# Kernel optimization log

Hardware: AMD Instinct MI355X
Metric: run time of the kernel (lower is better)

The kernel has to match this reference:

```python
import math
import jax, jax.numpy as jnp
import numpy as np

B, T_ALL, D = 128, 197, 768
T = T_ALL - 1
ORG, E, DFF, NCLS = 5, 8, 1024, 100
CAP_FACTOR = 1.25
MAX_K = 2  # training=True -> min(2, n_experts)


def setup_inputs() -> dict:
    key = jax.random.key(0)
    ks = jax.random.split(key, 16)
    s = lambda *sh: 0.02
    inp = {
        "tokens": jax.random.normal(ks[0], (B, T_ALL, D), jnp.float32),
        "organ_priors": jax.random.uniform(ks[1], (B, ORG), jnp.float32),
        "router_w": jax.random.normal(ks[2], (D + ORG, E), jnp.float32) * 0.02,
        "router_b": jnp.zeros((E,), jnp.float32),
        "w1": jax.random.normal(ks[3], (E, D, DFF), jnp.float32) * 0.02,
        "b1": jnp.zeros((E, DFF), jnp.float32),
        "w2": jax.random.normal(ks[4], (E, DFF, D), jnp.float32) * 0.02,
        "b2": jnp.zeros((E, D), jnp.float32),
        "ln_g": jnp.ones((D,), jnp.float32),
        "ln_b": jnp.zeros((D,), jnp.float32),
        "cls_w": jax.random.normal(ks[5], (D, NCLS), jnp.float32) * 0.02,
        "cls_b": jnp.zeros((NCLS,), jnp.float32),
        "aux_w": jax.random.normal(ks[6], (D, ORG), jnp.float32) * 0.02,
        "aux_b": jnp.zeros((ORG,), jnp.float32),
    }
    return inp


def switch_moe(flat, flat_prior, router_w, router_b, w1, b1, w2, b2):
    N = flat.shape[0]
    capacity = math.ceil(N / E * CAP_FACTOR)  # static
    logits = jnp.concatenate([flat, flat_prior], axis=-1) @ router_w + router_b  # (N,E)
    probs = jax.nn.softmax(logits, axis=-1)
    entropy = -(probs * jnp.log(probs + 1e-12)).sum(-1)  # (N,)
    topk_vals, topk_idx = jax.lax.top_k(probs, MAX_K)  # (N,K)
    topk_probs = topk_vals / (topk_vals.sum(-1, keepdims=True) + 1e-12)
    # one-hot expert assignment over top-k slots: (N,E)
    sel = jnp.any(topk_idx[:, None, :] == jnp.arange(E)[None, :, None], axis=-1)
    # combine weight per (token, expert): first (unique) matching top-k slot's prob
    w_full = (topk_probs[:, None, :] * (topk_idx[:, None, :] == jnp.arange(E)[None, :, None])).sum(-1)  # (N,E)
    # capacity-limited dispatch: per expert keep top-`capacity` tokens by router prob
    score = jnp.where(sel, probs, -jnp.inf).T  # (E,N)
    top_scores, idx = jax.lax.top_k(score, capacity)  # (E,cap), sorted desc like torch.sort
    valid = jnp.isfinite(top_scores)  # (E,cap)
    gathered = flat[idx]  # (E,cap,D)
    h = jax.nn.gelu(jnp.einsum('ecd,edf->ecf', gathered, w1) + b1[:, None, :], approximate=False)
    out_sel = jnp.einsum('ecf,efd->ecd', h, w2) + b2[:, None, :]  # (E,cap,D)
    w_sel = jnp.take_along_axis(w_full.T, idx, axis=1) * valid  # (E,cap)
    flat_idx = idx.reshape(-1)
    outputs = jnp.zeros_like(flat).at[flat_idx].add((out_sel * w_sel[..., None]).reshape(-1, D))
    processed = jnp.zeros((N,), jnp.float32).at[flat_idx].add(valid.reshape(-1).astype(jnp.float32)) > 0
    outputs = jnp.where(processed[:, None], outputs, flat)
    return outputs, probs, entropy


def reference(tokens, organ_priors, router_w, router_b, w1, b1, w2, b2,
              ln_g, ln_b, cls_w, cls_b, aux_w, aux_b):
    cls = tokens[:, 0, :]                # (B,D)
    patches = tokens[:, 1:, :]           # (B,T,D)
    flat = patches.reshape(B * T, D)
    flat_prior = jnp.broadcast_to(organ_priors[:, None, :], (B, T, ORG)).reshape(B * T, ORG)
    out_flat, probs, entropy = switch_moe(flat, flat_prior, router_w, router_b, w1, b1, w2, b2)
    # cls token passes through MoE untouched (only patches go through switch)
    mu = cls.mean(-1, keepdims=True)
    var = ((cls - mu) ** 2).mean(-1, keepdims=True)
    cls_final = (cls - mu) * jax.lax.rsqrt(var + 1e-5) * ln_g + ln_b
    logits = cls_final @ cls_w + cls_b
    aux_org = cls_final @ aux_w + aux_b
    return logits, aux_org, probs.reshape(B, T, E), entropy.reshape(B, T)
```

## Files before the change

kernel.cpp:

```cpp
#include <hip/hip_runtime.h>
#include <hip/hip_bf16.h>
#include <math.h>

#define NB     128
#define NT_ALL 197
#define NT     196
#define ND     768
#define NORG   5
#define NE     8
#define NCLS   100
#define NCOL   105
#define NTOK   (NB * NT)
#define KB     24
#define KHALF  12
#define XROW   776

#define RBLKS  784
#define CBLKS  256

typedef short  bf16x8 __attribute__((ext_vector_type(8)));
typedef float  f32x4  __attribute__((ext_vector_type(4)));


struct SharedRouter {
    __hip_bfloat16 x[32 * XROW];
    __hip_bfloat16 a[KB * 4 * 16 * 8];
    float pl[2][NE];
    float acc[2][64][4];
};
struct SharedCls {
    float x[ND];
    float red[4];
    float part[4][65];
};

__global__ __launch_bounds__(256, 4) void fused_kernel(
    const float* __restrict__ tokens,
    const float* __restrict__ priors,
    const float* __restrict__ rw,
    const float* __restrict__ rbias,
    const float* __restrict__ ln_g, const float* __restrict__ ln_b,
    const float* __restrict__ cls_w,
    const float* __restrict__ cls_b,
    const float* __restrict__ aux_w,
    const float* __restrict__ aux_b,
    float* __restrict__ out_logits,
    float* __restrict__ out_aux,
    float* __restrict__ probs_out,
    float* __restrict__ ent_out)
{
    __shared__ union { SharedRouter r; SharedCls c; } sm;
    const int t = threadIdx.x;

    if (blockIdx.x < RBLKS) {
        const int tok0 = blockIdx.x * 32;

#pragma unroll 6
        for (int i = t; i < 32 * ND / 4; i += 256) {
            const int tok = i / 192;
            const int k   = (i - tok * 192) * 4;
            const int gt  = tok0 + tok;
            const int b   = gt / NT;
            const float4 v = *reinterpret_cast<const float4*>(
                tokens + (size_t)(gt + b + 1) * ND + k);
            union { __hip_bfloat16 h[4]; ushort4 u; } pk;
            pk.h[0] = __float2bfloat16(v.x);
            pk.h[1] = __float2bfloat16(v.y);
            pk.h[2] = __float2bfloat16(v.z);
            pk.h[3] = __float2bfloat16(v.w);
            *reinterpret_cast<ushort4*>(&sm.r.x[tok * XROW + k]) = pk.u;
        }

        {
            bf16x8 z = {0, 0, 0, 0, 0, 0, 0, 0};
            bf16x8* p = (bf16x8*)sm.r.a;
            for (int i = t; i < KB * 4 * 8; i += 256)
                p[(i >> 3) * 16 + 8 + (i & 7)] = z;
        }
        for (int i = t; i < ND * NE; i += 256) {
            const int k = i >> 3, e = i & 7;
            const int kb = k >> 5, gg = (k >> 3) & 3, j = k & 7;
            sm.r.a[(((kb * 4 + gg) * 16) + e) * 8 + j] = __float2bfloat16(rw[i]);
        }
        const int b0 = tok0 / NT;
        const int b1 = (tok0 + 31) / NT;
        if (t < 16) {
            const int e = t & 7, which = t >> 3;
            const int bb = which ? b1 : b0;
            float a = rbias[e];
#pragma unroll
            for (int o = 0; o < NORG; ++o)
                a = fmaf(priors[bb * NORG + o], rw[(ND + o) * NE + e], a);
            sm.r.pl[which][e] = a;
        }
        __syncthreads();

        const int wid  = t >> 6;
        const int lane = t & 63;
        const int pair = wid >> 1;
        const int half = wid & 1;
        const int tt   = lane & 15;
        const int g    = lane >> 4;
        const int token = tok0 + pair * 16 + tt;
        const int b  = token / NT;

        const bf16x8* s_a8 =
            (const bf16x8*)sm.r.a + (half * KHALF * 4 + g) * 16 + tt;
        const __hip_bfloat16* xrow =
            sm.r.x + (pair * 16 + tt) * XROW + half * (KHALF * 32) + g * 8;

        f32x4 acc0 = {0.f, 0.f, 0.f, 0.f};
        f32x4 acc1 = {0.f, 0.f, 0.f, 0.f};
#pragma unroll
        for (int kb = 0; kb < KHALF; ++kb) {
            const bf16x8 xf = *reinterpret_cast<const bf16x8*>(xrow + kb * 32);
            const bf16x8 af = s_a8[kb * 64];
            if (kb & 1)
                acc1 = __builtin_amdgcn_mfma_f32_16x16x32_bf16(af, xf, acc1, 0, 0, 0);
            else
                acc0 = __builtin_amdgcn_mfma_f32_16x16x32_bf16(af, xf, acc0, 0, 0, 0);
        }
        f32x4 acc = acc0 + acc1;

        if (half == 1)
            *reinterpret_cast<f32x4*>(&sm.r.acc[pair][lane][0]) = acc;
        __syncthreads();

        if (half == 0) {
            acc += *reinterpret_cast<const f32x4*>(&sm.r.acc[pair][lane][0]);

            const float p0 = __shfl_xor(acc[0], 16, 64);
            const float p1 = __shfl_xor(acc[1], 16, 64);
            const float p2 = __shfl_xor(acc[2], 16, 64);
            const float p3 = __shfl_xor(acc[3], 16, 64);

            if (lane < 16) {
                float lg[NE] = {acc[0], acc[1], acc[2], acc[3], p0, p1, p2, p3};
                const int bsel = (b == b0) ? 0 : 1;
#pragma unroll
                for (int e = 0; e < NE; ++e) lg[e] += sm.r.pl[bsel][e];

                float m = lg[0];
#pragma unroll
                for (int e = 1; e < NE; ++e) m = fmaxf(m, lg[e]);
                float S = 0.f, dd = 0.f;
#pragma unroll
                for (int e = 0; e < NE; ++e) {
                    const float l = lg[e] - m;
                    const float p = __expf(l);
                    lg[e] = p;
                    S += p;
                    dd = fmaf(p, l, dd);
                }
                const float inv = 1.f / S;
                const float ent = __logf(S) - dd * inv;

                float4 q0 = {lg[0] * inv, lg[1] * inv, lg[2] * inv, lg[3] * inv};
                float4 q1 = {lg[4] * inv, lg[5] * inv, lg[6] * inv, lg[7] * inv};
                *reinterpret_cast<float4*>(probs_out + (size_t)token * NE)     = q0;
                *reinterpret_cast<float4*>(probs_out + (size_t)token * NE + 4) = q1;
                ent_out[token] = ent;
            }
        }
    } else {
        const int cb   = blockIdx.x - RBLKS;
        const int b    = cb >> 1;
        const int half = cb & 1;
        const int lane = t & 63;
        const int wv   = t >> 6;

        const float* xp = tokens + (size_t)b * NT_ALL * ND;

        float sum = 0.f;
        for (int i = t; i < ND; i += 256) { float v = xp[i]; sm.c.x[i] = v; sum += v; }
#pragma unroll
        for (int off = 32; off; off >>= 1) sum += __shfl_xor(sum, off, 64);
        if (lane == 0) sm.c.red[wv] = sum;
        __syncthreads();
        const float mu = (sm.c.red[0] + sm.c.red[1] + sm.c.red[2] + sm.c.red[3]) * (1.f / ND);
        __syncthreads();

        float sq = 0.f;
        for (int i = t; i < ND; i += 256) { float d = sm.c.x[i] - mu; sq += d * d; }
#pragma unroll
        for (int off = 32; off; off >>= 1) sq += __shfl_xor(sq, off, 64);
        if (lane == 0) sm.c.red[wv] = sq;
        __syncthreads();
        const float var  = (sm.c.red[0] + sm.c.red[1] + sm.c.red[2] + sm.c.red[3]) * (1.f / ND);
        const float rstd = rsqrtf(var + 1e-5f);
        __syncthreads();

        for (int i = t; i < ND; i += 256)
            sm.c.x[i] = (sm.c.x[i] - mu) * rstd * ln_g[i] + ln_b[i];
        __syncthreads();

        const int c = half * 64 + lane;
        const float* wp; int st;
        if (c < NCLS)      { wp = cls_w + c;          st = NCLS; }
        else if (c < NCOL) { wp = aux_w + (c - NCLS); st = NORG; }
        else               { wp = aux_w;              st = NORG; }

        const int d0 = wv * 192;
        const float* w = wp + (size_t)d0 * st;
        const int st2 = 2 * st, st3 = 3 * st, st4 = 4 * st;
        float a0 = 0.f, a1 = 0.f, a2 = 0.f, a3 = 0.f;
#pragma unroll 8
        for (int j = 0; j < 192; j += 4) {
            const float4 x4 = *reinterpret_cast<const float4*>(&sm.c.x[d0 + j]);
            a0 = fmaf(x4.x, w[0],   a0);
            a1 = fmaf(x4.y, w[st],  a1);
            a2 = fmaf(x4.z, w[st2], a2);
            a3 = fmaf(x4.w, w[st3], a3);
            w += st4;
        }
        sm.c.part[wv][lane] = (a0 + a1) + (a2 + a3);
        __syncthreads();

        if (t < 64) {
            float r = sm.c.part[0][t] + sm.c.part[1][t] + sm.c.part[2][t] + sm.c.part[3][t];
            const int cc = half * 64 + t;
            if (cc < NCLS)
                out_logits[b * NCLS + cc] = r + cls_b[cc];
            else if (cc < NCOL)
                out_aux[b * NORG + (cc - NCLS)] = r + aux_b[cc - NCLS];
        }
    }
}

extern "C" void kernel_launch(void* const* d_in, const int* in_sizes, int n_in,
                              void* d_out, int out_size, void* d_ws, size_t ws_size,
                              hipStream_t stream) {
    const float* tokens = (const float*)d_in[0];
    const float* priors = (const float*)d_in[1];
    const float* rw     = (const float*)d_in[2];
    const float* rbias  = (const float*)d_in[3];
    const float* ln_g   = (const float*)d_in[8];
    const float* ln_b   = (const float*)d_in[9];
    const float* cls_w  = (const float*)d_in[10];
    const float* cls_b  = (const float*)d_in[11];
    const float* aux_w  = (const float*)d_in[12];
    const float* aux_b  = (const float*)d_in[13];

    float* out = (float*)d_out;
    float* out_logits = out;
    float* out_aux    = out + NB * NCLS;
    float* out_probs  = out + NB * NCLS + NB * NORG;
    float* out_ent    = out + NB * NCLS + NB * NORG + (size_t)NTOK * NE;

    fused_kernel<<<RBLKS + CBLKS, 256, 0, stream>>>(
        tokens, priors, rw, rbias, ln_g, ln_b, cls_w, cls_b, aux_w, aux_b,
        out_logits, out_aux, out_probs, out_ent);
}
```

Baseline: 26.87 us.

## Load router tokens via async global-to-LDS DMA with swizzle, 16 tokens per block

Token rows are now copied straight from global memory into LDS as fp32 with global_load_lds and an XOR swizzle, and converted to bf16 when read for the MFMA. This replaces the register round trip of load, convert and store. Each block now handles 16 tokens with the K dimension split four ways across waves, so twice as many blocks run, and the launch bound drops to 2 blocks per CU because the fp32 tile needs more LDS. The router weight staging is also vectorised with float4 loads. The aim is to cut staging overhead and improve memory-level parallelism, at the cost of lower occupancy and a four-way cross-wave reduction.

```diff
diff --git a/kernel.cpp b/kernel.cpp
--- a/kernel.cpp
+++ b/kernel.cpp
@@ -12,10 +12,9 @@
 #define NCOL   105
 #define NTOK   (NB * NT)
 #define KB     24
-#define KHALF  12
-#define XROW   776
-
-#define RBLKS  784
+#define KQ     6
+
+#define RBLKS  1568
 #define CBLKS  256
 
 typedef short  bf16x8 __attribute__((ext_vector_type(8)));
@@ -23,10 +22,10 @@
 
 
 struct SharedRouter {
-    __hip_bfloat16 x[32 * XROW];
+    float x[16 * ND];
     __hip_bfloat16 a[KB * 4 * 16 * 8];
+    float acc[3][64][4];
     float pl[2][NE];
-    float acc[2][64][4];
 };
 struct SharedCls {
     float x[ND];
@@ -34,7 +33,14 @@
     float part[4][65];
 };
 
-__global__ __launch_bounds__(256, 4) void fused_kernel(
+__device__ __forceinline__ void dma16(const void* g, void* l) {
+    __builtin_amdgcn_global_load_lds(
+        (const __attribute__((address_space(1))) void*)g,
+        (__attribute__((address_space(3))) void*)l,
+        16, 0, 0);
+}
+
+__global__ __launch_bounds__(256, 2) void fused_kernel(
     const float* __restrict__ tokens,
     const float* __restrict__ priors,
     const float* __restrict__ rw,
@@ -53,22 +59,20 @@
     const int t = threadIdx.x;
 
     if (blockIdx.x < RBLKS) {
-        const int tok0 = blockIdx.x * 32;
-
-#pragma unroll 6
-        for (int i = t; i < 32 * ND / 4; i += 256) {
-            const int tok = i / 192;
-            const int k   = (i - tok * 192) * 4;
-            const int gt  = tok0 + tok;
-            const int b   = gt / NT;
-            const float4 v = *reinterpret_cast<const float4*>(
-                tokens + (size_t)(gt + b + 1) * ND + k);
-            union { __hip_bfloat16 h[4]; ushort4 u; } pk;
-            pk.h[0] = __float2bfloat16(v.x);
-            pk.h[1] = __float2bfloat16(v.y);
-            pk.h[2] = __float2bfloat16(v.z);
-            pk.h[3] = __float2bfloat16(v.w);
-            *reinterpret_cast<ushort4*>(&sm.r.x[tok * XROW + k]) = pk.u;
+        const int wid  = t >> 6;
+        const int lane = t & 63;
+        const int tok0 = blockIdx.x * 16;
+
+#pragma unroll
+        for (int i = 0; i < 12; ++i) {
+            const int ltt = wid * 4 + i / 3;
+            const int s0  = (i % 3) * 1024;
+            const int gt  = tok0 + ltt;
+            const int bb  = gt / NT;
+            const size_t rowb = (size_t)(gt + bb + 1) * (ND * 4);
+            const int soff = (s0 + lane * 16) ^ ((ltt & 7) << 4);
+            dma16((const char*)tokens + rowb + soff,
+                  (char*)sm.r.x + ltt * 3072 + s0);
         }
 
         {
@@ -77,13 +81,22 @@
             for (int i = t; i < KB * 4 * 8; i += 256)
                 p[(i >> 3) * 16 + 8 + (i & 7)] = z;
         }
-        for (int i = t; i < ND * NE; i += 256) {
-            const int k = i >> 3, e = i & 7;
+        for (int k = t; k < ND; k += 256) {
+            const float4 w0 = *reinterpret_cast<const float4*>(rw + k * 8);
+            const float4 w1 = *reinterpret_cast<const float4*>(rw + k * 8 + 4);
             const int kb = k >> 5, gg = (k >> 3) & 3, j = k & 7;
-            sm.r.a[(((kb * 4 + gg) * 16) + e) * 8 + j] = __float2bfloat16(rw[i]);
+            __hip_bfloat16* dst = &sm.r.a[((kb * 4 + gg) * 16) * 8 + j];
+            dst[0 * 8] = __float2bfloat16(w0.x);
+            dst[1 * 8] = __float2bfloat16(w0.y);
+            dst[2 * 8] = __float2bfloat16(w0.z);
+            dst[3 * 8] = __float2bfloat16(w0.w);
+            dst[4 * 8] = __float2bfloat16(w1.x);
+            dst[5 * 8] = __float2bfloat16(w1.y);
+            dst[6 * 8] = __float2bfloat16(w1.z);
+            dst[7 * 8] = __float2bfloat16(w1.w);
         }
         const int b0 = tok0 / NT;
-        const int b1 = (tok0 + 31) / NT;
+        const int b1 = (tok0 + 15) / NT;
         if (t < 16) {
             const int e = t & 7, which = t >> 3;
             const int bb = which ? b1 : b0;
@@ -95,39 +108,45 @@
         }
         __syncthreads();
 
-        const int wid  = t >> 6;
-        const int lane = t & 63;
-        const int pair = wid >> 1;
-        const int half = wid & 1;
-        const int tt   = lane & 15;
-        const int g    = lane >> 4;
-        const int token = tok0 + pair * 16 + tt;
-        const int b  = token / NT;
-
-        const bf16x8* s_a8 =
-            (const bf16x8*)sm.r.a + (half * KHALF * 4 + g) * 16 + tt;
-        const __hip_bfloat16* xrow =
-            sm.r.x + (pair * 16 + tt) * XROW + half * (KHALF * 32) + g * 8;
+        const int tt  = lane & 15;
+        const int g   = lane >> 4;
+        const int swz = (tt & 7) << 4;
+        const char* xbase = (const char*)sm.r.x + tt * 3072;
+        const bf16x8* s_a8 = (const bf16x8*)sm.r.a;
 
         f32x4 acc0 = {0.f, 0.f, 0.f, 0.f};
         f32x4 acc1 = {0.f, 0.f, 0.f, 0.f};
 #pragma unroll
-        for (int kb = 0; kb < KHALF; ++kb) {
-            const bf16x8 xf = *reinterpret_cast<const bf16x8*>(xrow + kb * 32);
-            const bf16x8 af = s_a8[kb * 64];
-            if (kb & 1)
-                acc1 = __builtin_amdgcn_mfma_f32_16x16x32_bf16(af, xf, acc1, 0, 0, 0);
+        for (int k = 0; k < KQ; ++k) {
+            const int kb   = wid * KQ + k;
+            const int koff = kb * 128 + g * 32;
+            const f32x4 xa = *reinterpret_cast<const f32x4*>(xbase + (koff ^ swz));
+            const f32x4 xc = *reinterpret_cast<const f32x4*>(xbase + ((koff + 16) ^ swz));
+            union { bf16x8 v; __hip_bfloat16 h[8]; } u;
+            u.h[0] = __float2bfloat16(xa[0]);
+            u.h[1] = __float2bfloat16(xa[1]);
+            u.h[2] = __float2bfloat16(xa[2]);
+            u.h[3] = __float2bfloat16(xa[3]);
+            u.h[4] = __float2bfloat16(xc[0]);
+            u.h[5] = __float2bfloat16(xc[1]);
+            u.h[6] = __float2bfloat16(xc[2]);
+            u.h[7] = __float2bfloat16(xc[3]);
+            const bf16x8 af = s_a8[(kb * 4 + g) * 16 + tt];
+            if (k & 1)
+                acc1 = __builtin_amdgcn_mfma_f32_16x16x32_bf16(af, u.v, acc1, 0, 0, 0);
             else
-                acc0 = __builtin_amdgcn_mfma_f32_16x16x32_bf16(af, xf, acc0, 0, 0, 0);
+                acc0 = __builtin_amdgcn_mfma_f32_16x16x32_bf16(af, u.v, acc0, 0, 0, 0);
         }
         f32x4 acc = acc0 + acc1;
 
-        if (half == 1)
-            *reinterpret_cast<f32x4*>(&sm.r.acc[pair][lane][0]) = acc;
-        __syncthreads();
-
-        if (half == 0) {
-            acc += *reinterpret_cast<const f32x4*>(&sm.r.acc[pair][lane][0]);
+        if (wid > 0)
+            *reinterpret_cast<f32x4*>(&sm.r.acc[wid - 1][lane][0]) = acc;
+        __syncthreads();
+
+        if (wid == 0) {
+            acc += *reinterpret_cast<const f32x4*>(&sm.r.acc[0][lane][0]);
+            acc += *reinterpret_cast<const f32x4*>(&sm.r.acc[1][lane][0]);
+            acc += *reinterpret_cast<const f32x4*>(&sm.r.acc[2][lane][0]);
 
             const float p0 = __shfl_xor(acc[0], 16, 64);
             const float p1 = __shfl_xor(acc[1], 16, 64);
@@ -135,6 +154,8 @@
             const float p3 = __shfl_xor(acc[3], 16, 64);
 
             if (lane < 16) {
+                const int token = tok0 + tt;
+                const int b = token / NT;
                 float lg[NE] = {acc[0], acc[1], acc[2], acc[3], p0, p1, p2, p3};
                 const int bsel = (b == b0) ? 0 : 1;
 #pragma unroll
```

New measurement: 29.76 us. 1.11x slower.
